# Kernel tuning notes

Measured on AMD Instinct MI355X. Metric: run time of the kernel, lower is better.

Reference implementation:

```python
import jax, jax.numpy as jnp
import numpy as np

B, C, T, I, R = 32, 4, 512, 64, 1024
LEAK = 0.5          # reak_rate
DENSITY = 0.1       # reservoir_density
SPECTRAL_RADIUS = 0.95
W_SCALE = 1.0       # reservoir_weights_scale
IN_SCALE = 0.1      # input_weights_scale


def setup_inputs() -> dict:
    rng = np.random.default_rng(0)
    # reservoir weights: uniform, sparsified by density mask, rescaled so the
    # largest singular value equals the target spectral radius (as in __init__)
    W = rng.uniform(-W_SCALE, W_SCALE, (R, R)).astype(np.float32)
    mask = (rng.uniform(0.0, 1.0, (R, R)) < DENSITY).astype(np.float32)
    W = W * mask
    s_max = np.linalg.svd(W, compute_uv=False).max()
    W = W * (SPECTRAL_RADIUS / s_max)
    # input weights: [R, I*C]
    Wi = rng.uniform(-IN_SCALE, IN_SCALE, (R, I * C)).astype(np.float32)

    key = jax.random.key(0)
    x = jax.random.normal(key, (B, C, T, I), dtype=jnp.float32)
    return {
        "x": x,
        "input_weights": jnp.asarray(Wi),
        "reservoir_weights": jnp.asarray(W),
    }


def reference(x, input_weights, reservoir_weights):
    # x: [B, C, T, I]
    B_, C_, T_, I_ = x.shape
    R_ = reservoir_weights.shape[0]
    # precompute the input projection for all steps: u_t = flatten(x[:,:,t,:]) @ Wi.T
    xt = jnp.transpose(x, (2, 0, 1, 3)).reshape(T_, B_, C_ * I_)  # [T, B, C*I]
    U = xt @ input_weights.T                                       # [T, B, R]

    h0 = jnp.zeros((B_, C_, R_), dtype=x.dtype)  # per-channel reservoir state

    def step(h, u):
        # leaky-integrated reservoir update; input broadcasts over channels
        h_new = LEAK * jnp.tanh(u[:, None, :] + h @ reservoir_weights) + (1.0 - LEAK) * h
        return h_new, h_new

    _, hs = jax.lax.scan(step, h0, U)            # hs: [T, B, C, R]
    return jnp.transpose(hs, (1, 2, 0, 3))       # [B, C, T, R]
```

## Files before the change

kernel.cpp:

```cpp
#include <hip/hip_runtime.h>
#include <hip/hip_bf16.h>
#include <cstdint>
#include <cstddef>


typedef unsigned short u16;
typedef unsigned int   u32;
typedef unsigned long long u64;
typedef __bf16 bf16x8 __attribute__((ext_vector_type(8)));
typedef u64    u64x2  __attribute__((ext_vector_type(2)));
typedef float  f32x4  __attribute__((ext_vector_type(4)));
typedef float  f32x2  __attribute__((ext_vector_type(2)));

#define T_STEPS 512
#define NWG     256
#define TPB     256

#define OFF_WHI 0
#define OFF_U   (2*1024*1024)
#define OFF_HB  (OFF_U + (size_t)512*32*1024*4)
#define HB_BYTES ((size_t)128*2048)
#define OFF_BAR (OFF_HB + 2*HB_BYTES)

__device__ __forceinline__ u16 f2bf(float f) {
  u32 u = __builtin_bit_cast(u32, f);
  u += 0x7fffu + ((u >> 16) & 1u);
  return (u16)(u >> 16);
}
__device__ __forceinline__ void pinv(bf16x8& v) { asm volatile("" : "+v"(v)); }

__device__ __forceinline__ u32 AADD(u32* p, u32 v) {
  return __hip_atomic_fetch_add(p, v, __ATOMIC_RELAXED, __HIP_MEMORY_SCOPE_AGENT);
}
__device__ __forceinline__ u32 ALD(const u32* p) {
  return __hip_atomic_load(p, __ATOMIC_RELAXED, __HIP_MEMORY_SCOPE_AGENT);
}
__device__ __forceinline__ u64 ALD64(const u64* p) {
  return __hip_atomic_load(p, __ATOMIC_RELAXED, __HIP_MEMORY_SCOPE_AGENT);
}
__device__ __forceinline__ void AST(u32* p, u32 v) {
  __hip_atomic_store(p, v, __ATOMIC_RELAXED, __HIP_MEMORY_SCOPE_AGENT);
}

__global__ void prep_w(const float* __restrict__ W, u16* __restrict__ whi) {
  int n = blockIdx.y;
  int k = blockIdx.x * 256 + threadIdx.x;
  whi[n * 1024 + k] = f2bf(W[k * 1024 + n]);
}

__global__ void prep_u(const float* __restrict__ x, const float* __restrict__ Wi,
                       float* __restrict__ U) {
  __shared__ float wi_t[256][64];
  __shared__ float xt[32][256];
  const int b = blockIdx.x, nt = blockIdx.y, tid = threadIdx.x;
  {
    int n = tid >> 2, jc = (tid & 3) * 64;
    const float* src = Wi + (size_t)(nt * 64 + n) * 256 + jc;
#pragma unroll
    for (int i = 0; i < 64; i += 4) {
      float4 v = *(const float4*)(src + i);
      wi_t[jc + i + 0][n] = v.x; wi_t[jc + i + 1][n] = v.y;
      wi_t[jc + i + 2][n] = v.z; wi_t[jc + i + 3][n] = v.w;
    }
  }
  const int wv = tid >> 6, nn = tid & 63;
  for (int tc = 0; tc < 16; ++tc) {
    __syncthreads();
    for (int s = 0; s < 8; ++s) {
      int fi = s * 256 + tid;
      int tt = fi >> 6, j4 = (fi & 63) * 4;
      int c = j4 >> 6, i = j4 & 63;
      float4 v = *(const float4*)(x + ((size_t)((b * 4 + c) * 512) + tc * 32 + tt) * 64 + i);
      *(float4*)&xt[tt][j4] = v;
    }
    __syncthreads();
    float acc[8] = {0,0,0,0,0,0,0,0};
    for (int j4 = 0; j4 < 64; ++j4) {
      float w0 = wi_t[j4 * 4 + 0][nn], w1 = wi_t[j4 * 4 + 1][nn];
      float w2 = wi_t[j4 * 4 + 2][nn], w3 = wi_t[j4 * 4 + 3][nn];
#pragma unroll
      for (int tt = 0; tt < 8; ++tt) {
        float4 xv = *(const float4*)&xt[wv * 8 + tt][j4 * 4];
        acc[tt] += xv.x * w0 + xv.y * w1 + xv.z * w2 + xv.w * w3;
      }
    }
#pragma unroll
    for (int tt = 0; tt < 8; ++tt)
      U[((size_t)(tc * 32 + wv * 8 + tt) * 32 + b) * 1024 + nt * 64 + nn] = acc[tt];
  }
}

__global__ void __launch_bounds__(TPB, 1) esn_scan(
    const u16* __restrict__ Whi, const float* __restrict__ U,
    u16* __restrict__ Hb, float* __restrict__ out, u32* __restrict__ bar) {
  __shared__ __align__(16) float red[8 * 64 * 4];
  __shared__ int sh_q, sh_j, sh_loc;

  const int tid = threadIdx.x;
  const int wv = tid >> 6, lane = tid & 63;
  const int mcol = lane & 15, kb = lane >> 4;

  if (tid == 0) {
    int xcd;
    asm volatile("s_getreg_b32 %0, hwreg(HW_REG_XCC_ID)" : "=s"(xcd));
    xcd &= 7;
    AADD(bar + xcd * 64, 1u);
    AADD(bar + 512, 1u);
    while (ALD(bar + 512) < (u32)NWG) __builtin_amdgcn_s_sleep(2);
    bool uni = true;
    for (int k = 0; k < 8; ++k) uni &= (ALD(bar + k * 64) == 32u);
    if (uni) {
      sh_q = xcd;
      sh_j = (int)AADD(bar + (9 + xcd) * 64, 1u);
      sh_loc = 1;
    } else {
      sh_q = blockIdx.x & 7;
      sh_j = blockIdx.x >> 3;
      sh_loc = 0;
    }
  }
  __syncthreads();
  const int q = sh_q, j = sh_j;
  const bool xlocal = (sh_loc != 0);
  const int r0 = q << 4, c0 = j << 5;

  bf16x8 bh[2][8];
#pragma unroll
  for (int nt = 0; nt < 2; ++nt) {
    const char* wb = (const char*)Whi + (size_t)(c0 + nt * 16 + mcol) * 2048
                     + wv * 512 + kb * 16;
#pragma unroll
    for (int kt = 0; kt < 8; ++kt)
      bh[nt][kt] = *(const bf16x8*)(wb + kt * 64);
  }
#pragma unroll
  for (int nt = 0; nt < 2; ++nt)
#pragma unroll
    for (int kt = 0; kt < 8; ++kt) pinv(bh[nt][kt]);

  const int row_l = tid >> 4;
  const int col0  = (tid & 15) * 2;
  const int grow  = r0 + row_l;
  const int ont   = col0 >> 4, oci = col0 & 15;
  const int okb   = row_l >> 2, orr = row_l & 3;
  u32* flags = bar + 2048 + q * 64;

  float hreg[2] = {0.f, 0.f};
  f32x2 uf = *(const f32x2*)(U + (size_t)(grow >> 2) * 1024 + c0 + col0);

  for (int t = 0; t < T_STEPS; ++t) {
    const char* hsrc = (const char*)Hb + (size_t)(t & 1) * HB_BYTES
                       + (size_t)(r0 + mcol) * 2048 + wv * 512 + kb * 16;
    bf16x8 av[8];
    if (xlocal) {
#pragma unroll
      for (int kt = 0; kt < 8; ++kt)
        av[kt] = *(const bf16x8*)(hsrc + kt * 64);
    } else {
#pragma unroll
      for (int kt = 0; kt < 8; ++kt) {
        u64x2 p;
        p.x = ALD64((const u64*)(hsrc + kt * 64));
        p.y = ALD64((const u64*)(hsrc + kt * 64 + 8));
        av[kt] = __builtin_bit_cast(bf16x8, p);
      }
    }

    f32x4 acc0 = {0.f, 0.f, 0.f, 0.f};
    f32x4 acc1 = {0.f, 0.f, 0.f, 0.f};
#pragma unroll
    for (int kt = 0; kt < 8; ++kt) {
      acc0 = __builtin_amdgcn_mfma_f32_16x16x32_bf16(av[kt], bh[0][kt], acc0, 0, 0, 0);
      acc1 = __builtin_amdgcn_mfma_f32_16x16x32_bf16(av[kt], bh[1][kt], acc1, 0, 0, 0);
    }

    *(f32x4*)&red[((wv * 2 + 0) * 64 + lane) * 4] = acc0;
    *(f32x4*)&red[((wv * 2 + 1) * 64 + lane) * 4] = acc1;
    __syncthreads();

    float z0 = 0.f, z1 = 0.f;
#pragma unroll
    for (int w = 0; w < 4; ++w) {
      z0 += red[((w * 2 + ont) * 64 + okb * 16 + oci + 0) * 4 + orr];
      z1 += red[((w * 2 + ont) * 64 + okb * 16 + oci + 1) * 4 + orr];
    }
    float hn0 = 0.5f * tanhf(z0 + uf.x) + 0.5f * hreg[0];
    float hn1 = 0.5f * tanhf(z1 + uf.y) + 0.5f * hreg[1];
    hreg[0] = hn0; hreg[1] = hn1;

    {
      u32 pk = (u32)f2bf(hn0) | ((u32)f2bf(hn1) << 16);
      u32* hdst = (u32*)((char*)Hb + (size_t)((t + 1) & 1) * HB_BYTES
                         + (size_t)grow * 2048 + (c0 + col0) * 2);
      if (xlocal) {
        *hdst = pk;
      } else {
        (void)__hip_atomic_exchange(hdst, pk, __ATOMIC_RELAXED,
                                    __HIP_MEMORY_SCOPE_AGENT);
      }
    }
    asm volatile("s_waitcnt vmcnt(0)" ::: "memory");
    __syncthreads();

    if (t < T_STEPS - 1) {
      if (tid == 0) {
        if (xlocal) *(volatile u32*)(flags + j) = (u32)(t + 1);
        else        AST(flags + j, (u32)(t + 1));
      }
    }

    {
      f32x2 o2; o2.x = hn0; o2.y = hn1;
      __builtin_nontemporal_store(o2,
          (f32x2*)(out + ((size_t)grow * 512 + t) * 1024 + c0 + col0));
    }
    if (t < T_STEPS - 1) {
      uf = *(const f32x2*)(U + ((size_t)(t + 1) * 32 + (grow >> 2)) * 1024 + c0 + col0);
      if (wv == 0) {
        u32 tgt = (u32)(t + 1);
        if (xlocal) {
          volatile const u32* f = (volatile const u32*)flags;
          while (true) {
            asm volatile("buffer_inv" ::: "memory");
            u32 v = f[lane & 31];
            if (__all(v >= tgt)) break;
            __builtin_amdgcn_s_sleep(1);
          }
        } else {
          while (true) {
            u32 v = ALD(flags + (lane & 31));
            if (__all(v >= tgt)) break;
            __builtin_amdgcn_s_sleep(1);
          }
        }
      }
      __syncthreads();
    }
  }
}

extern "C" void kernel_launch(void* const* d_in, const int* in_sizes, int n_in,
                              void* d_out, int out_size, void* d_ws, size_t ws_size,
                              hipStream_t stream) {
  (void)in_sizes; (void)n_in; (void)out_size; (void)ws_size;
  const float* x  = (const float*)d_in[0];
  const float* Wi = (const float*)d_in[1];
  const float* W  = (const float*)d_in[2];
  float* out = (float*)d_out;

  char* ws  = (char*)d_ws;
  u16*  whi = (u16*)(ws + OFF_WHI);
  float* U  = (float*)(ws + OFF_U);
  u16*  hb  = (u16*)(ws + OFF_HB);
  u32*  bar = (u32*)(ws + OFF_BAR);

  (void)hipMemsetAsync(ws + OFF_HB, 0, 2 * HB_BYTES + 16384, stream);

  hipLaunchKernelGGL(prep_w, dim3(4, 1024), dim3(256), 0, stream, W, whi);
  hipLaunchKernelGGL(prep_u, dim3(32, 16), dim3(256), 0, stream, x, Wi, U);
  hipLaunchKernelGGL(esn_scan, dim3(NWG), dim3(TPB), 0, stream,
                     whi, U, hb, out, bar);
}
```

Measured before the change: 1.690 ms.

## Compute input projection with split-bf16 MFMA and tighten scan flag polling

Replaces the scalar FP32 input-projection kernel with an MFMA GEMM. It splits x and Wi into bf16 hi/lo parts and uses three MFMAs per tile to keep near-fp32 accuracy, staging x in swizzled shared memory. The scan's local-XCD flag wait now spins on an atomic load without sleeping and issues one buffer_inv after the wait, instead of invalidating the cache on every poll. The costs are extra conversion arithmetic, a small accuracy change from the hi/lo split, and more memory traffic from busy polling.

Measured after the change: 1.419 ms. 1.19x faster.

```diff
diff --git a/kernel.cpp b/kernel.cpp
--- a/kernel.cpp
+++ b/kernel.cpp
@@ -27,6 +27,10 @@
   u += 0x7fffu + ((u >> 16) & 1u);
   return (u16)(u >> 16);
 }
+__device__ __forceinline__ float bf2f(u16 h) {
+  u32 u = ((u32)h) << 16;
+  return __builtin_bit_cast(float, u);
+}
 __device__ __forceinline__ void pinv(bf16x8& v) { asm volatile("" : "+v"(v)); }
 
 __device__ __forceinline__ u32 AADD(u32* p, u32 v) {
@@ -48,45 +52,91 @@
   whi[n * 1024 + k] = f2bf(W[k * 1024 + n]);
 }
 
-__global__ void prep_u(const float* __restrict__ x, const float* __restrict__ Wi,
-                       float* __restrict__ U) {
-  __shared__ float wi_t[256][64];
-  __shared__ float xt[32][256];
-  const int b = blockIdx.x, nt = blockIdx.y, tid = threadIdx.x;
-  {
-    int n = tid >> 2, jc = (tid & 3) * 64;
-    const float* src = Wi + (size_t)(nt * 64 + n) * 256 + jc;
-#pragma unroll
-    for (int i = 0; i < 64; i += 4) {
-      float4 v = *(const float4*)(src + i);
-      wi_t[jc + i + 0][n] = v.x; wi_t[jc + i + 1][n] = v.y;
-      wi_t[jc + i + 2][n] = v.z; wi_t[jc + i + 3][n] = v.w;
-    }
-  }
-  const int wv = tid >> 6, nn = tid & 63;
-  for (int tc = 0; tc < 16; ++tc) {
+__global__ void __launch_bounds__(256) prep_u2(const float* __restrict__ x,
+                                               const float* __restrict__ Wi,
+                                               float* __restrict__ U) {
+  __shared__ __align__(16) u16 Ah[128 * 128];
+  __shared__ __align__(16) u16 Al[128 * 128];
+  const int tid = threadIdx.x;
+  const int m0 = blockIdx.x << 7;
+  const int n0 = blockIdx.y << 7;
+  const int wv = tid >> 6, lane = tid & 63;
+  const int fc = lane & 15, kb = lane >> 4;
+
+  f32x4 acc[8][2];
+#pragma unroll
+  for (int mt = 0; mt < 8; ++mt) {
+    acc[mt][0] = (f32x4){0.f, 0.f, 0.f, 0.f};
+    acc[mt][1] = (f32x4){0.f, 0.f, 0.f, 0.f};
+  }
+
+  for (int hf = 0; hf < 2; ++hf) {
     __syncthreads();
-    for (int s = 0; s < 8; ++s) {
-      int fi = s * 256 + tid;
-      int tt = fi >> 6, j4 = (fi & 63) * 4;
-      int c = j4 >> 6, i = j4 & 63;
-      float4 v = *(const float4*)(x + ((size_t)((b * 4 + c) * 512) + tc * 32 + tt) * 64 + i);
-      *(float4*)&xt[tt][j4] = v;
+#pragma unroll
+    for (int s = 0; s < 16; ++s) {
+      int f = (s << 8) + tid;
+      int row = f >> 5, v = f & 31;
+      int cl = v >> 4, i4 = (v & 15) << 2;
+      int b = row & 31, t = (m0 + row) >> 5;
+      float4 xv = *(const float4*)(x +
+          ((size_t)((b << 2) | ((hf << 1) | cl)) * 512 + t) * 64 + i4);
+      int byte = (row << 8) + (((cl << 7) + (i4 << 1)) ^ ((row & 7) << 4));
+      u16* ph = (u16*)((char*)Ah + byte);
+      u16* pl = (u16*)((char*)Al + byte);
+      float vv[4] = {xv.x, xv.y, xv.z, xv.w};
+#pragma unroll
+      for (int e = 0; e < 4; ++e) {
+        u16 hh = f2bf(vv[e]);
+        ph[e] = hh;
+        pl[e] = f2bf(vv[e] - bf2f(hh));
+      }
+    }
+    bf16x8 Bh[2][4], Bl[2][4];
+#pragma unroll
+    for (int nt = 0; nt < 2; ++nt) {
+      const float* wrow = Wi + (size_t)(n0 + (wv << 5) + (nt << 4) + fc) * 256;
+#pragma unroll
+      for (int kt = 0; kt < 4; ++kt) {
+        int k = (hf << 7) + (kt << 5) + (kb << 3);
+        float tmp[8];
+        *(float4*)&tmp[0] = *(const float4*)(wrow + k);
+        *(float4*)&tmp[4] = *(const float4*)(wrow + k + 4);
+#pragma unroll
+        for (int e = 0; e < 8; ++e) {
+          u16 hh = f2bf(tmp[e]);
+          Bh[nt][kt][e] = __builtin_bit_cast(__bf16, hh);
+          Bl[nt][kt][e] = __builtin_bit_cast(__bf16, f2bf(tmp[e] - bf2f(hh)));
+        }
+      }
     }
     __syncthreads();
-    float acc[8] = {0,0,0,0,0,0,0,0};
-    for (int j4 = 0; j4 < 64; ++j4) {
-      float w0 = wi_t[j4 * 4 + 0][nn], w1 = wi_t[j4 * 4 + 1][nn];
-      float w2 = wi_t[j4 * 4 + 2][nn], w3 = wi_t[j4 * 4 + 3][nn];
-#pragma unroll
-      for (int tt = 0; tt < 8; ++tt) {
-        float4 xv = *(const float4*)&xt[wv * 8 + tt][j4 * 4];
-        acc[tt] += xv.x * w0 + xv.y * w1 + xv.z * w2 + xv.w * w3;
-      }
-    }
-#pragma unroll
-    for (int tt = 0; tt < 8; ++tt)
-      U[((size_t)(tc * 32 + wv * 8 + tt) * 32 + b) * 1024 + nt * 64 + nn] = acc[tt];
+#pragma unroll
+    for (int kt = 0; kt < 4; ++kt) {
+      int kbyte = (kt << 6) + (kb << 4);
+#pragma unroll
+      for (int mt = 0; mt < 8; ++mt) {
+        int row = (mt << 4) + fc;
+        int byte = (row << 8) + (kbyte ^ ((row & 7) << 4));
+        bf16x8 ah = *(const bf16x8*)((char*)Ah + byte);
+        bf16x8 al = *(const bf16x8*)((char*)Al + byte);
+#pragma unroll
+        for (int nt = 0; nt < 2; ++nt) {
+          acc[mt][nt] = __builtin_amdgcn_mfma_f32_16x16x32_bf16(ah, Bh[nt][kt], acc[mt][nt], 0, 0, 0);
+          acc[mt][nt] = __builtin_amdgcn_mfma_f32_16x16x32_bf16(al, Bh[nt][kt], acc[mt][nt], 0, 0, 0);
+          acc[mt][nt] = __builtin_amdgcn_mfma_f32_16x16x32_bf16(ah, Bl[nt][kt], acc[mt][nt], 0, 0, 0);
+        }
+      }
+    }
+  }
+#pragma unroll
+  for (int mt = 0; mt < 8; ++mt) {
+    int mbase = m0 + (mt << 4) + (kb << 2);
+    int n = n0 + (wv << 5) + fc;
+#pragma unroll
+    for (int nt = 0; nt < 2; ++nt)
+#pragma unroll
+      for (int r = 0; r < 4; ++r)
+        U[(size_t)(mbase + r) * 1024 + n + (nt << 4)] = acc[mt][nt][r];
   }
 }
 
@@ -219,17 +269,16 @@
       if (wv == 0) {
         u32 tgt = (u32)(t + 1);
         if (xlocal) {
-          volatile const u32* f = (volatile const u32*)flags;
+          const u32* fp = flags + (lane & 31);
           while (true) {
-            asm volatile("buffer_inv" ::: "memory");
-            u32 v = f[lane & 31];
-            if (__all(v >= tgt)) break;
-            __builtin_amdgcn_s_sleep(1);
+            u32 v = ALD(fp);
+            if (__all((int)(v >= tgt))) break;
           }
+          asm volatile("buffer_inv\n\ts_waitcnt vmcnt(0)" ::: "memory");
         } else {
           while (true) {
             u32 v = ALD(flags + (lane & 31));
-            if (__all(v >= tgt)) break;
+            if (__all((int)(v >= tgt))) break;
             __builtin_amdgcn_s_sleep(1);
           }
         }
@@ -257,7 +306,7 @@
   (void)hipMemsetAsync(ws + OFF_HB, 0, 2 * HB_BYTES + 16384, stream);
 
   hipLaunchKernelGGL(prep_w, dim3(4, 1024), dim3(256), 0, stream, W, whi);
-  hipLaunchKernelGGL(prep_u, dim3(32, 16), dim3(256), 0, stream, x, Wi, U);
+  hipLaunchKernelGGL(prep_u2, dim3(128, 8), dim3(256), 0, stream, x, Wi, U);
   hipLaunchKernelGGL(esn_scan, dim3(NWG), dim3(TPB), 0, stream,
                      whi, U, hb, out, bar);
 }
```
